# Kernel tuning notes

Measured on AMD Instinct MI355X. Metric: run time of the kernel, lower is better.

Reference implementation:

```python
import jax, jax.numpy as jnp
import numpy as np

B, S, D = 2, 2048, 2048
HK, HV = 16, 32
DK, DV = 128, 128
KDIM = HK * DK          # 2048
VDIM = HV * DV          # 4096
CONV_DIM = 2 * KDIM + VDIM  # 8192
KSIZE = 4
EPS = 1e-6


def setup_inputs() -> dict:
    key = jax.random.key(0)
    ks = jax.random.split(key, 10)
    w = lambda i, shape, sc=0.02: jax.random.normal(ks[i], shape, jnp.float32) * sc
    return {
        "hidden_states": jax.random.normal(ks[0], (B, S, D), jnp.float32),
        "w_qkv": w(1, (D, CONV_DIM)),
        "w_z": w(2, (D, VDIM)),
        "w_b": w(3, (D, HV)),
        "w_a": w(4, (D, HV)),
        "w_out": w(5, (VDIM, D)),
        "conv_w": w(6, (CONV_DIM, KSIZE), 0.2),   # depthwise conv kernel [C, K]
        "dt_bias": jnp.ones((HV,), jnp.float32),
        "A_log": jnp.log(jax.random.uniform(ks[7], (HV,), jnp.float32, 1e-3, 16.0)),
        "norm_weight": jnp.ones((DV,), jnp.float32),
    }


def _causal_conv1d(x, w):
    # x: [B,S,C], w: [C,K] depthwise; left-pad K-1 zeros -> causal, output len S
    xp = jnp.pad(x, ((0, 0), (KSIZE - 1, 0), (0, 0)))
    lhs = xp.transpose(0, 2, 1)            # [B,C,S+K-1]
    rhs = w[:, None, :]                    # [C,1,K]
    out = jax.lax.conv_general_dilated(lhs, rhs, (1,), 'VALID',
                                       feature_group_count=CONV_DIM)
    return out.transpose(0, 2, 1)          # [B,S,C]


def _l2norm(x, eps=1e-6):
    return x * jax.lax.rsqrt(jnp.sum(x * x, axis=-1, keepdims=True) + eps)


def _gated_delta_rule(q, k, v, g, beta):
    # q,k: [B,S,H,DK]; v: [B,S,H,DV]; g,beta: [B,S,H]
    q = q * (DK ** -0.5)

    def step(St, inp):
        q_t, k_t, v_t, g_t, b_t = inp      # [B,H,dk], [B,H,dk], [B,H,dv], [B,H], [B,H]
        St = St * jnp.exp(g_t)[..., None, None]             # per-head decay
        v_old = jnp.einsum('bhk,bhkv->bhv', k_t, St)        # read memory
        delta = (v_t - v_old) * b_t[..., None]              # delta-rule update
        St = St + k_t[..., None] * delta[:, :, None, :]     # write memory
        o = jnp.einsum('bhk,bhkv->bhv', q_t, St)            # read output
        return St, o

    tr = lambda x: jnp.moveaxis(x, 1, 0)  # seq-major for scan
    S0 = jnp.zeros((q.shape[0], HV, DK, DV), jnp.float32)
    _, out = jax.lax.scan(step, S0, (tr(q), tr(k), tr(v), tr(g), tr(beta)))
    return jnp.moveaxis(out, 0, 1)         # [B,S,H,DV]


def reference(hidden_states, w_qkv, w_z, w_b, w_a, w_out, conv_w,
              dt_bias, A_log, norm_weight):
    Bb, Ss, _ = hidden_states.shape
    mixed = hidden_states @ w_qkv                           # [B,S,CONV_DIM]
    z = (hidden_states @ w_z).reshape(Bb, Ss, HV, DV)
    b = hidden_states @ w_b                                 # [B,S,HV]
    a = hidden_states @ w_a                                 # [B,S,HV]

    mixed = jax.nn.silu(_causal_conv1d(mixed, conv_w))
    q, k, v = jnp.split(mixed, [KDIM, 2 * KDIM], axis=-1)
    q = _l2norm(q.reshape(Bb, Ss, HK, DK))
    k = _l2norm(k.reshape(Bb, Ss, HK, DK))
    v = v.reshape(Bb, Ss, HV, DV)

    beta = jax.nn.sigmoid(b)
    g = -jnp.exp(A_log) * jax.nn.softplus(a + dt_bias)      # [B,S,HV]

    rep = HV // HK
    q = jnp.repeat(q, rep, axis=2)
    k = jnp.repeat(k, rep, axis=2)

    core = _gated_delta_rule(q, k, v, g, beta)              # [B,S,HV,DV]

    # gated RMSNorm over DV: norm(x)*weight*silu(gate)
    var = jnp.mean(core * core, axis=-1, keepdims=True)
    core = core * jax.lax.rsqrt(var + EPS) * norm_weight
    core = core * jax.nn.silu(z)

    return core.reshape(Bb, Ss, VDIM) @ w_out               # [B,S,D]
```

## Files before the change

### kernel.cpp

```cpp
#include <hip/hip_runtime.h>
#include <hip/hip_bf16.h>
#include <cstdint>
#include <cstddef>


typedef __bf16 bf16;
typedef __bf16 bf16x8 __attribute__((ext_vector_type(8)));
typedef __bf16 bf16x4v __attribute__((ext_vector_type(4)));
typedef float f32x4 __attribute__((ext_vector_type(4)));

#define NB 2
#define NS 2048
#define ND 2048
#define NHK 16
#define NHV 32
#define NDK 128
#define NDV 128
#define NKDIM 2048
#define NVDIM 4096
#define NCONV 8192

__device__ __forceinline__ bool detect_f32(const void* dt_raw) {
  return ((const uint32_t*)dt_raw)[0] == 0x3F800000u;
}
__device__ __forceinline__ float inval(const void* p, size_t i, bool f32in) {
  return f32in ? ((const float*)p)[i] : (float)((const bf16*)p)[i];
}

__device__ __forceinline__ void gload_lds16(const bf16* gp, bf16* lp) {
  typedef __attribute__((address_space(1))) const void gvoid_t;
  typedef __attribute__((address_space(3))) void lvoid_t;
  __builtin_amdgcn_global_load_lds((gvoid_t*)gp, (lvoid_t*)lp, 16, 0, 0);
}

__global__ __launch_bounds__(256) void convert_hs(const void* __restrict__ in,
    const void* __restrict__ dt_raw, bf16* __restrict__ out)
{
  const bool f32in = detect_f32(dt_raw);
  const size_t base = (size_t)(blockIdx.x * 256 + threadIdx.x) * 8;
  bf16x8 o;
#pragma unroll
  for (int j = 0; j < 8; j++) o[j] = (bf16)inval(in, base + j, f32in);
  *(bf16x8*)(out + base) = o;
}

__global__ __launch_bounds__(256) void convert_small(const void* __restrict__ conv_w,
    const void* __restrict__ dt_bias, const void* __restrict__ A_log,
    const void* __restrict__ norm_w, bf16* __restrict__ conv_wB,
    float* __restrict__ dtf, float* __restrict__ alogf, float* __restrict__ normwf)
{
  const bool f32in = detect_f32(dt_bias);
  const int idx = blockIdx.x * 256 + threadIdx.x;
  if (idx < 32768)      conv_wB[idx] = (bf16)inval(conv_w, idx, f32in);
  else if (idx < 32800) dtf[idx - 32768]   = inval(dt_bias, idx - 32768, f32in);
  else if (idx < 32832) alogf[idx - 32800] = inval(A_log, idx - 32800, f32in);
  else if (idx < 32960) normwf[idx - 32832] = inval(norm_w, idx - 32832, f32in);
}

template <bool F32OUT>
__global__ __launch_bounds__(256) void gemm_bt(const bf16* __restrict__ A,
    const bf16* __restrict__ Bt, void* __restrict__ Cv, int M, int N, int K)
{
  __shared__ bf16 As[128 * 32];
  __shared__ bf16 Bs[128 * 32];
  const int tid  = threadIdx.x;
  const int lane = tid & 63;
  const int wave = tid >> 6;
  const int wr = wave >> 1, wc = wave & 1;
  const int l15 = lane & 15, quad = lane >> 4;
  const int bm = blockIdx.y * 128;
  const int bn = blockIdx.x * 128;

  f32x4 acc[4][4];
#pragma unroll
  for (int i = 0; i < 4; i++)
#pragma unroll
    for (int j = 0; j < 4; j++)
      acc[i][j] = (f32x4){0.f, 0.f, 0.f, 0.f};

  const int li0 = wave * 128 + lane;
  const int li1 = li0 + 64;
  const int r0 = li0 >> 2, c0 = (li0 & 3) * 8;
  const int r1 = li1 >> 2, c1 = (li1 & 3) * 8;

  for (int k0 = 0; k0 < K; k0 += 32) {
    gload_lds16(A  + (size_t)(bm + r0) * K + k0 + c0, &As[(wave * 2 + 0) * 512]);
    gload_lds16(A  + (size_t)(bm + r1) * K + k0 + c1, &As[(wave * 2 + 1) * 512]);
    gload_lds16(Bt + (size_t)(bn + r0) * K + k0 + c0, &Bs[(wave * 2 + 0) * 512]);
    gload_lds16(Bt + (size_t)(bn + r1) * K + k0 + c1, &Bs[(wave * 2 + 1) * 512]);
    __syncthreads();
    bf16x8 af[4], bfr[4];
#pragma unroll
    for (int mi = 0; mi < 4; mi++)
      af[mi] = *(const bf16x8*)&As[(wr * 64 + mi * 16 + l15) * 32 + quad * 8];
#pragma unroll
    for (int ni = 0; ni < 4; ni++)
      bfr[ni] = *(const bf16x8*)&Bs[(wc * 64 + ni * 16 + l15) * 32 + quad * 8];
#pragma unroll
    for (int mi = 0; mi < 4; mi++)
#pragma unroll
      for (int ni = 0; ni < 4; ni++)
        acc[mi][ni] = __builtin_amdgcn_mfma_f32_16x16x32_bf16(af[mi], bfr[ni], acc[mi][ni], 0, 0, 0);
    __syncthreads();
  }
#pragma unroll
  for (int mi = 0; mi < 4; mi++)
#pragma unroll
    for (int ni = 0; ni < 4; ni++)
#pragma unroll
      for (int r = 0; r < 4; r++) {
        const int row = bm + wr * 64 + mi * 16 + quad * 4 + r;
        const int col = bn + wc * 64 + ni * 16 + l15;
        if (F32OUT)
          ((float*)Cv)[(size_t)row * N + col] = acc[mi][ni][r];
        else
          ((bf16*)Cv)[(size_t)row * N + col] = (bf16)acc[mi][ni][r];
      }
}

__global__ __launch_bounds__(256) void transpose_k(const void* __restrict__ in,
    const void* __restrict__ dt_raw, bf16* __restrict__ out, int K, int N)
{
  const bool f32in = detect_f32(dt_raw);
  __shared__ bf16 tile[32][33];
  const int n0 = blockIdx.x * 32, k0 = blockIdx.y * 32;
  const int x = threadIdx.x, y0 = threadIdx.y;
#pragma unroll
  for (int i = 0; i < 4; i++) {
    int y = y0 + i * 8;
    tile[y][x] = (bf16)inval(in, (size_t)(k0 + y) * N + n0 + x, f32in);
  }
  __syncthreads();
#pragma unroll
  for (int i = 0; i < 4; i++) {
    int y = y0 + i * 8;
    out[(size_t)(n0 + y) * K + k0 + x] = tile[x][y];
  }
}

__global__ __launch_bounds__(256) void build_wba(const void* __restrict__ w_b,
    const void* __restrict__ w_a, const void* __restrict__ dt_raw,
    bf16* __restrict__ wbaT)
{
  const bool f32in = detect_f32(dt_raw);
  const int idx = blockIdx.x * 256 + threadIdx.x;
  const int n = idx >> 11, k = idx & 2047;
  bf16 v = (bf16)0.f;
  if (n < 32) v = (bf16)inval(w_b, (size_t)k * 32 + n, f32in);
  else if (n < 64) v = (bf16)inval(w_a, (size_t)k * 32 + (n - 32), f32in);
  wbaT[idx] = v;
}

__global__ __launch_bounds__(256) void betag_kernel(const bf16* __restrict__ ba,
    const float* __restrict__ dtf, const float* __restrict__ alogf,
    float* __restrict__ g, float* __restrict__ beta)
{
  const int idx = blockIdx.x * 256 + threadIdx.x;
  const int tok = idx >> 6, j = idx & 63;
  const float d = (float)ba[(size_t)tok * 128 + j];
  if (j < 32) {
    beta[(size_t)tok * 32 + j] = 1.f / (1.f + expf(-d));
  } else {
    const int h = j - 32;
    const float x = d + dtf[h];
    const float sp = (x > 20.f) ? x : log1pf(expf(x));
    g[(size_t)tok * 32 + h] = -expf(alogf[h]) * sp;
  }
}

__global__ __launch_bounds__(256) void conv_kernel(const bf16* __restrict__ mixed,
    const bf16* __restrict__ conv_w, bf16* __restrict__ qhat,
    bf16* __restrict__ khat, bf16* __restrict__ vout)
{
  const int blk = blockIdx.x;
  const int b = blk >> 11, s = blk & 2047;
  const int t = threadIdx.x;
  __shared__ float ssq[512];
  __shared__ float rn[32];
  float vals[4][8];
#pragma unroll
  for (int i = 0; i < 4; i++) {
    const int vg = t + 256 * i;
    const int c = vg * 8;
    const bf16x8* wp = (const bf16x8*)(conv_w + (size_t)c * 4);
    const bf16x8 w0 = wp[0], w1 = wp[1], w2 = wp[2], w3 = wp[3];
    float acc[8] = {0.f, 0.f, 0.f, 0.f, 0.f, 0.f, 0.f, 0.f};
#pragma unroll
    for (int l = 0; l < 4; l++) {
      const int ss = s - 3 + l;
      if (ss >= 0) {
        const bf16x8 x8 = *(const bf16x8*)(mixed + (size_t)(b * 2048 + ss) * NCONV + c);
#pragma unroll
        for (int j = 0; j < 8; j++) {
          const int widx = j * 4 + l;
          const float wv = (widx < 8)  ? (float)w0[widx]
                         : (widx < 16) ? (float)w1[widx - 8]
                         : (widx < 24) ? (float)w2[widx - 16]
                                       : (float)w3[widx - 24];
          acc[j] += (float)x8[j] * wv;
        }
      }
    }
    float lsq = 0.f;
#pragma unroll
    for (int j = 0; j < 8; j++) {
      const float x = acc[j];
      const float y = x / (1.f + expf(-x));
      vals[i][j] = y;
      lsq += y * y;
    }
    if (vg < 512) {
      ssq[vg] = lsq;
    } else {
      bf16x8 o;
#pragma unroll
      for (int j = 0; j < 8; j++) o[j] = (bf16)vals[i][j];
      *(bf16x8*)(vout + (size_t)(b * 2048 + s) * NVDIM + (c - 4096)) = o;
    }
  }
  __syncthreads();
  if (t < 32) {
    float sum = 0.f;
#pragma unroll
    for (int u = 0; u < 16; u++) sum += ssq[t * 16 + u];
    float r = rsqrtf(sum + 1e-6f);
    if (t < 16) r *= 0.08838834764831845f;
    rn[t] = r;
  }
  __syncthreads();
#pragma unroll
  for (int i = 0; i < 2; i++) {
    const int vg = t + 256 * i;
    const float sc = rn[vg >> 4];
    bf16x8 o;
#pragma unroll
    for (int j = 0; j < 8; j++) o[j] = (bf16)(vals[i][j] * sc);
    if (vg < 256)
      *(bf16x8*)(qhat + (size_t)(b * 2048 + s) * NKDIM + vg * 8) = o;
    else
      *(bf16x8*)(khat + (size_t)(b * 2048 + s) * NKDIM + (vg - 256) * 8) = o;
  }
}

__global__ __launch_bounds__(256) void prep_kernel(const bf16* __restrict__ qhat,
    const bf16* __restrict__ khat, bf16* __restrict__ vbuf,
    const float* __restrict__ g, const float* __restrict__ beta,
    bf16* __restrict__ Wg, bf16* __restrict__ Mg, float* __restrict__ egG,
    float* __restrict__ sc2G, float* __restrict__ egTotG)
{
  const int bid = blockIdx.x;
  const int c = bid & 127;
  const int h = (bid >> 7) & 31;
  const int b = bid >> 12;
  const int qh = h >> 1;
  const int s0 = c * 16;
  const int t = threadIdx.x;
  const int wave = t >> 6, lane = t & 63;
  const int l15 = lane & 15, quad = lane >> 4;
  const int sidx = t >> 4, seg = t & 15;

  __shared__ __attribute__((aligned(16))) bf16 pK[16 * 136];
  __shared__ __attribute__((aligned(16))) bf16 pQ[16 * 136];
  __shared__ __attribute__((aligned(16))) bf16 pV[16 * 136];
  __shared__ float sA[16 * 17];
  __shared__ float sGc[16], sEg[16], sBt[16];

  const f32x4 zero4 = (f32x4){0.f, 0.f, 0.f, 0.f};

  {
    const size_t kb = ((size_t)(b * 2048 + s0 + sidx) * NHK + qh) * NDK + seg * 8;
    *(bf16x8*)&pK[sidx * 136 + seg * 8] = *(const bf16x8*)(khat + kb);
    *(bf16x8*)&pQ[sidx * 136 + seg * 8] = *(const bf16x8*)(qhat + kb);
    const size_t vb = ((size_t)(b * 2048 + s0 + sidx) * NHV + h) * NDV + seg * 8;
    *(bf16x8*)&pV[sidx * 136 + seg * 8] = *(const bf16x8*)(vbuf + vb);
  }
  if (wave == 0) {
    float gb_r = 0.f;
    if (lane < 16)      gb_r = g[(size_t)(b * 2048 + s0 + lane) * NHV + h];
    else if (lane < 32) gb_r = beta[(size_t)(b * 2048 + s0 + (lane - 16)) * NHV + h];
    float gc = gb_r;
#pragma unroll
    for (int off = 1; off < 16; off <<= 1) {
      const float n = __shfl_up(gc, off);
      if ((lane & 15) >= off) gc += n;
    }
    const float gtot = __shfl(gc, 15);
    if (lane < 16) {
      sGc[lane] = gc;
      const float e = expf(gc);
      sEg[lane] = e;
      const float s2 = expf(gtot - gc);
      egG[(size_t)bid * 16 + lane] = e;
      sc2G[(size_t)bid * 16 + lane] = s2;
      if (lane == 15) egTotG[bid] = e;
    } else if (lane < 32) {
      sBt[lane - 16] = gb_r;
    }
  }
  __syncthreads();

  f32x4 accKK = zero4, accQK = zero4;
  if (wave == 0) {
#pragma unroll
    for (int kk = 0; kk < 4; kk++) {
      const bf16x8 af = *(const bf16x8*)&pK[l15 * 136 + kk * 32 + quad * 8];
      accKK = __builtin_amdgcn_mfma_f32_16x16x32_bf16(af, af, accKK, 0, 0, 0);
    }
#pragma unroll
    for (int r = 0; r < 4; r++) {
      const int tt = quad * 4 + r, ii = l15;
      float a = 0.f;
      if (ii < tt) a = sBt[tt] * expf(sGc[tt] - sGc[ii]) * accKK[r];
      sA[tt * 17 + ii] = a;
    }
  } else if (wave == 1) {
#pragma unroll
    for (int kk = 0; kk < 4; kk++) {
      const bf16x8 af = *(const bf16x8*)&pQ[l15 * 136 + kk * 32 + quad * 8];
      const bf16x8 bf_ = *(const bf16x8*)&pK[l15 * 136 + kk * 32 + quad * 8];
      accQK = __builtin_amdgcn_mfma_f32_16x16x32_bf16(af, bf_, accQK, 0, 0, 0);
    }
#pragma unroll
    for (int r = 0; r < 4; r++) {
      const int tt = quad * 4 + r, ii = l15;
      const float m = (ii <= tt) ? expf(sGc[tt] - sGc[ii]) * accQK[r] : 0.f;
      Mg[(size_t)bid * 512 + tt * 32 + ii] = (bf16)m;
      Mg[(size_t)bid * 512 + tt * 32 + 16 + ii] = (bf16)0.f;
    }
  }
  __syncthreads();

  {
    const int j = t;
    float x[16];
#pragma unroll
    for (int tt = 0; tt < 16; tt++) {
      float r = (j < 128) ? sBt[tt] * sEg[tt] * (float)pK[tt * 136 + j]
                          : sBt[tt] * (float)pV[tt * 136 + (j - 128)];
#pragma unroll
      for (int i = 0; i < 16; i++)
        if (i < tt) r = fmaf(-sA[tt * 17 + i], x[i], r);
      x[tt] = r;
    }
    if (j < 128) {
#pragma unroll
      for (int tt = 0; tt < 16; tt++)
        Wg[(size_t)bid * 2048 + tt * 128 + j] = (bf16)x[tt];
    } else {
#pragma unroll
      for (int tt = 0; tt < 16; tt++)
        vbuf[((size_t)(b * 2048 + s0 + tt) * NHV + h) * NDV + (j - 128)] = (bf16)x[tt];
    }
  }
}

__global__ __launch_bounds__(256, 2) void core_kernel(const bf16* __restrict__ qhat,
    const bf16* __restrict__ khat, const bf16* __restrict__ Ug,
    const bf16* __restrict__ Wg, const bf16* __restrict__ Mg,
    const float* __restrict__ egG, const float* __restrict__ sc2G,
    const float* __restrict__ egTotG, bf16* __restrict__ corep)
{
  const int bid = blockIdx.x;
  const int vblk = (bid & 7) * 64 + (bid >> 3);
  const int dvc = vblk & 7;
  const int h = (vblk >> 3) & 31;
  const int b = vblk >> 8;
  const int qh = h >> 1;
  const int dvbase = dvc * 16;
  const int t = threadIdx.x;
  const int wave = t >> 6, lane = t & 63;
  const int l15 = lane & 15, quad = lane >> 4;
  const int sidx = t >> 4, seg = t & 15;
  const size_t cb = (size_t)(b * 32 + h) * 128;

  __shared__ __attribute__((aligned(16))) bf16 sKb[2][16 * 136];
  __shared__ __attribute__((aligned(16))) bf16 sKT[128 * 40];
  __shared__ __attribute__((aligned(16))) bf16 sSt[2][16 * 136];
  __shared__ __attribute__((aligned(16))) bf16 sD[16 * 40];
  __shared__ __attribute__((aligned(16))) bf16 sD2[16 * 40];

  const f32x4 zero4 = (f32x4){0.f, 0.f, 0.f, 0.f};
  for (int i = t; i < 272; i += 256) {
    *(f32x4*)&sSt[0][i * 8] = zero4;
    *(f32x4*)&sSt[1][i * 8] = zero4;
  }
  for (int i = t; i < 80; i += 256) {
    *(f32x4*)&sD[i * 8] = zero4;
    *(f32x4*)&sD2[i * 8] = zero4;
  }
  for (int i = t; i < 640; i += 256) *(f32x4*)&sKT[i * 8] = zero4;

  f32x4 accS[2] = {zero4, zero4};

  const int swz = (l15 & 7) << 3;

  bf16x8 kv_r;
  bf16x8 wf[4]; float u4[4], sc2_4[4];
  bf16x8 qf[4], mf; float eg_4[4];
  float egTot_r;

  auto load_kv = [&](int c) {
    const int cc = c < 128 ? c : 127;
    kv_r = *(const bf16x8*)(khat +
        ((size_t)(b * 2048 + cc * 16 + sidx) * NHK + qh) * NDK + seg * 8);
  };
  auto load_w0 = [&](int c) {
    const int cc = c < 128 ? c : 127;
    const size_t wb = (cb + cc) * 2048 + (size_t)l15 * 128 + quad * 8;
#pragma unroll
    for (int kk = 0; kk < 4; kk++) wf[kk] = *(const bf16x8*)(Wg + wb + kk * 32);
#pragma unroll
    for (int r = 0; r < 4; r++) {
      u4[r] = (float)Ug[((size_t)(b * 2048 + cc * 16 + quad * 4 + r) * NHV + h) * NDV
                        + dvbase + l15];
      sc2_4[r] = sc2G[(cb + cc) * 16 + quad * 4 + r];
    }
  };
  auto load_qf = [&](int c) {
    const int cc = c < 128 ? c : 127;
    const size_t qb = ((size_t)(b * 2048 + cc * 16 + l15) * NHK + qh) * NDK + quad * 8;
#pragma unroll
    for (int kk = 0; kk < 4; kk++) qf[kk] = *(const bf16x8*)(qhat + qb + kk * 32);
  };
  auto load_w1m = [&](int c) {
    const int cc = c < 128 ? c : 127;
    mf = *(const bf16x8*)(Mg + (cb + cc) * 512 + l15 * 32 + quad * 8);
#pragma unroll
    for (int r = 0; r < 4; r++) eg_4[r] = egG[(cb + cc) * 16 + quad * 4 + r];
  };
  auto load_egtot = [&](int c) { egTot_r = egTotG[cb + (c < 128 ? c : 127)]; };

  load_kv(0);
  *(bf16x8*)&sKb[0][sidx * 136 + seg * 8] = kv_r;
  load_kv(1);
  if (wave == 0) load_w0(0);
  else if (wave == 1) { load_qf(0); load_w1m(0); }
  load_egtot(0);
  __syncthreads();

#pragma unroll 1
  for (int ch = 0; ch < 128; ++ch) {
    const int cur = ch & 1, nxt = cur ^ 1;
    const int s0 = ch * 16;
    f32x4 accO = zero4;
    if (wave == 0) {
      f32x4 aH = zero4, aL = zero4;
#pragma unroll
      for (int kk = 0; kk < 4; kk++) {
        const int col = (kk * 32 + quad * 8) ^ swz;
        const bf16x8 sh = *(const bf16x8*)&sSt[0][l15 * 136 + col];
        const bf16x8 sl = *(const bf16x8*)&sSt[1][l15 * 136 + col];
        aH = __builtin_amdgcn_mfma_f32_16x16x32_bf16(wf[kk], sh, aH, 0, 0, 0);
        aL = __builtin_amdgcn_mfma_f32_16x16x32_bf16(wf[kk], sl, aL, 0, 0, 0);
      }
      bf16x4v d4, d24;
#pragma unroll
      for (int r = 0; r < 4; r++) {
        const float d = u4[r] - (aH[r] + aL[r]);
        d4[r] = (bf16)d;
        d24[r] = (bf16)(d * sc2_4[r]);
      }
      *(bf16x4v*)&sD[l15 * 40 + quad * 4] = d4;
      *(bf16x4v*)&sD2[l15 * 40 + quad * 4] = d24;
      load_w0(ch + 1);
    } else if (wave == 1) {
      f32x4 aH = zero4, aL = zero4;
#pragma unroll
      for (int kk = 0; kk < 4; kk++) {
        const int col = (kk * 32 + quad * 8) ^ swz;
        const bf16x8 sh = *(const bf16x8*)&sSt[0][l15 * 136 + col];
        const bf16x8 sl = *(const bf16x8*)&sSt[1][l15 * 136 + col];
        aH = __builtin_amdgcn_mfma_f32_16x16x32_bf16(qf[kk], sh, aH, 0, 0, 0);
        aL = __builtin_amdgcn_mfma_f32_16x16x32_bf16(qf[kk], sl, aL, 0, 0, 0);
      }
#pragma unroll
      for (int r = 0; r < 4; r++) accO[r] = eg_4[r] * (aH[r] + aL[r]);
      load_qf(ch + 1);
    } else {
      const int dk_w = (wave - 2) * 64 + lane;
#pragma unroll
      for (int ih = 0; ih < 2; ih++) {
        bf16x8 kt;
#pragma unroll
        for (int j = 0; j < 8; j++) kt[j] = sKb[cur][(ih * 8 + j) * 136 + dk_w];
        *(bf16x8*)&sKT[dk_w * 40 + ih * 8] = kt;
      }
    }
    __syncthreads();
    *(bf16x8*)&sKb[nxt][sidx * 136 + seg * 8] = kv_r;
    load_kv(ch + 2);
    if (wave == 1) {
      const bf16x8 bD = *(const bf16x8*)&sD[l15 * 40 + quad * 8];
      accO = __builtin_amdgcn_mfma_f32_16x16x32_bf16(mf, bD, accO, 0, 0, 0);
#pragma unroll
      for (int r = 0; r < 4; r++)
        corep[((size_t)(b * 2048 + s0 + quad * 4 + r) * NHV + h) * NDV + dvbase + l15]
            = (bf16)accO[r];
      load_w1m(ch + 1);
    }
    {
      const bf16x8 bD2 = *(const bf16x8*)&sD2[l15 * 40 + quad * 8];
#pragma unroll
      for (int ti = 0; ti < 2; ti++) {
        const int dk0 = wave * 32 + ti * 16;
        const bf16x8 kf = *(const bf16x8*)&sKT[(dk0 + l15) * 40 + quad * 8];
        accS[ti] = accS[ti] * egTot_r;
        accS[ti] = __builtin_amdgcn_mfma_f32_16x16x32_bf16(kf, bD2, accS[ti], 0, 0, 0);
      }
      load_egtot(ch + 1);
#pragma unroll
      for (int ti = 0; ti < 2; ti++) {
        const int dk0 = wave * 32 + ti * 16;
        bf16x4v hi4, lo4;
#pragma unroll
        for (int r = 0; r < 4; r++) {
          const float v = accS[ti][r];
          const bf16 hi = (bf16)v;
          hi4[r] = hi;
          lo4[r] = (bf16)(v - (float)hi);
        }
        const int col = (dk0 + quad * 4) ^ swz;
        *(bf16x4v*)&sSt[0][l15 * 136 + col] = hi4;
        *(bf16x4v*)&sSt[1][l15 * 136 + col] = lo4;
      }
    }
    __syncthreads();
  }
}

__global__ __launch_bounds__(128) void normgate_kernel(const bf16* __restrict__ core,
    const bf16* __restrict__ z, const float* __restrict__ normwf,
    bf16* __restrict__ gated)
{
  const size_t idx = blockIdx.x;
  const int t = threadIdx.x;
  const float x = (float)core[idx * 128 + t];
  float p = x * x;
#pragma unroll
  for (int off = 32; off > 0; off >>= 1) p += __shfl_down(p, off);
  __shared__ float s2[2];
  if ((t & 63) == 0) s2[t >> 6] = p;
  __syncthreads();
  const float var = (s2[0] + s2[1]) * (1.f / 128.f);
  const float zv = (float)z[idx * 128 + t];
  const float y = x * rsqrtf(var + 1e-6f) * normwf[t] * (zv / (1.f + expf(-zv)));
  gated[idx * 128 + t] = (bf16)y;
}

extern "C" void kernel_launch(void* const* d_in, const int* in_sizes, int n_in,
                              void* d_out, int out_size, void* d_ws, size_t ws_size,
                              hipStream_t stream)
{
  const void* hs     = d_in[0];
  const void* w_qkv  = d_in[1];
  const void* w_z    = d_in[2];
  const void* w_b    = d_in[3];
  const void* w_a    = d_in[4];
  const void* w_out  = d_in[5];
  const void* conv_w = d_in[6];
  const void* dt_b   = d_in[7];
  const void* A_log  = d_in[8];
  const void* norm_w = d_in[9];

  char* ws = (char*)d_ws;
  bf16*  mixed = (bf16*)(ws + 0);
  bf16*  corep = (bf16*)(ws + 0);
  bf16*  Wg    = (bf16*)(ws + 33554432);
  bf16*  wqkvT = (bf16*)(ws + 67108864);
  bf16*  qhat  = (bf16*)(ws + 67108864);
  bf16*  khat  = (bf16*)(ws + 83886080);
  bf16*  gated = (bf16*)(ws + 67108864);
  bf16*  wzT   = (bf16*)(ws + 100663296);
  bf16*  woutT = (bf16*)(ws + 100663296);
  bf16*  vbuf  = (bf16*)(ws + 117440512);
  bf16*  zbuf  = (bf16*)(ws + 150994944);
  bf16*  hsB   = (bf16*)(ws + 184549376);
  bf16*  Mg    = (bf16*)(ws + 184549376);
  float* egG   = (float*)(ws + 192937984);
  float* sc2G  = (float*)(ws + 193462272);
  float* egTotG= (float*)(ws + 193986560);
  bf16*  wbaT  = (bf16*)(ws + 201326592);
  bf16*  ba    = (bf16*)(ws + 201850880);
  float* gb    = (float*)(ws + 202899456);
  float* betab = (float*)(ws + 203423744);
  bf16*  convwB= (bf16*)(ws + 203948032);
  float* dtf   = (float*)(ws + 204013568);
  float* alogf = (float*)(ws + 204013696);
  float* normwf= (float*)(ws + 204013824);

  convert_hs<<<4096, 256, 0, stream>>>(hs, dt_b, hsB);
  convert_small<<<129, 256, 0, stream>>>(conv_w, dt_b, A_log, norm_w,
                                         convwB, dtf, alogf, normwf);

  const dim3 tb(32, 8);
  transpose_k<<<dim3(NCONV / 32, ND / 32), tb, 0, stream>>>(w_qkv, dt_b, wqkvT, ND, NCONV);
  transpose_k<<<dim3(NVDIM / 32, ND / 32), tb, 0, stream>>>(w_z, dt_b, wzT, ND, NVDIM);
  build_wba<<<1024, 256, 0, stream>>>(w_b, w_a, dt_b, wbaT);

  gemm_bt<false><<<dim3(NCONV / 128, 32), 256, 0, stream>>>(hsB, wqkvT, mixed, 4096, NCONV, ND);
  gemm_bt<false><<<dim3(NVDIM / 128, 32), 256, 0, stream>>>(hsB, wzT, zbuf, 4096, NVDIM, ND);
  gemm_bt<false><<<dim3(1, 32), 256, 0, stream>>>(hsB, wbaT, ba, 4096, 128, ND);

  transpose_k<<<dim3(ND / 32, NVDIM / 32), tb, 0, stream>>>(w_out, dt_b, woutT, NVDIM, ND);

  betag_kernel<<<1024, 256, 0, stream>>>(ba, dtf, alogf, gb, betab);
  conv_kernel<<<NB * NS, 256, 0, stream>>>(mixed, convwB, qhat, khat, vbuf);
  prep_kernel<<<8192, 256, 0, stream>>>(qhat, khat, vbuf, gb, betab,
                                        Wg, Mg, egG, sc2G, egTotG);
  core_kernel<<<512, 256, 0, stream>>>(qhat, khat, vbuf, Wg, Mg,
                                       egG, sc2G, egTotG, corep);
  normgate_kernel<<<NB * NS * NHV, 128, 0, stream>>>(corep, zbuf, normwf, gated);

  gemm_bt<true><<<dim3(ND / 128, 32), 256, 0, stream>>>(gated, woutT, (void*)d_out, 4096, ND, NVDIM);
}
```

Measured before the change: 933.6 us.

## Replace projection GEMMs with 256x256-tile, 4-stage LDS-pipelined MFMA kernel

Adds a new GEMM kernel with 256x256 output tiles, 512 threads, a 4-deep buffer ring filled by direct global-to-LDS loads, an XCD-aware block remapping, and raised wave priority around the MFMA section. It replaces the old 128x128 GEMM for the qkv, z and output projections. The aim is more data reuse per tile and overlap of global loads with MFMA work. The larger LDS footprint and register tiles may limit occupancy, and the output projection grid has only 128 blocks, which may not fill the device.

```diff
diff --git a/kernel.cpp b/kernel.cpp
--- a/kernel.cpp
+++ b/kernel.cpp
@@ -55,6 +55,101 @@
   else if (idx < 32800) dtf[idx - 32768]   = inval(dt_bias, idx - 32768, f32in);
   else if (idx < 32832) alogf[idx - 32800] = inval(A_log, idx - 32800, f32in);
   else if (idx < 32960) normwf[idx - 32832] = inval(norm_w, idx - 32832, f32in);
+}
+
+template <bool F32OUT>
+__global__ __launch_bounds__(512, 2) void gemm256(const bf16* __restrict__ A,
+    const bf16* __restrict__ Bt, void* __restrict__ Cv, int M, int N, int K)
+{
+  const int nbx = N >> 8;
+  const int nwg = gridDim.x;
+  const int cpx = nwg >> 3;
+  const int wg = (blockIdx.x & 7) * cpx + (blockIdx.x >> 3);
+  const int bm = (wg / nbx) << 8;
+  const int bn = (wg % nbx) << 8;
+
+  const int t = threadIdx.x;
+  const int wave = t >> 6, lane = t & 63;
+  const int wm = wave >> 2, wn = wave & 3;
+  const int l15 = lane & 15, quad = lane >> 4;
+
+  __shared__ __attribute__((aligned(16))) bf16 sA[4][8192];
+  __shared__ __attribute__((aligned(16))) bf16 sB[4][8192];
+
+  const bf16* gA0 = A  + (size_t)(bm + (wave * 2 + 0) * 16 + l15) * K + quad * 8;
+  const bf16* gA1 = A  + (size_t)(bm + (wave * 2 + 1) * 16 + l15) * K + quad * 8;
+  const bf16* gB0 = Bt + (size_t)(bn + (wave * 2 + 0) * 16 + l15) * K + quad * 8;
+  const bf16* gB1 = Bt + (size_t)(bn + (wave * 2 + 1) * 16 + l15) * K + quad * 8;
+  const int sd0 = (wave * 2 + 0) * 512;
+  const int sd1 = (wave * 2 + 1) * 512;
+
+  auto STAGE = [&](int kt, int buf) {
+    const size_t off = (size_t)kt * 32;
+    gload_lds16(gA0 + off, &sA[buf][sd0]);
+    gload_lds16(gA1 + off, &sA[buf][sd1]);
+    gload_lds16(gB0 + off, &sB[buf][sd0]);
+    gload_lds16(gB1 + off, &sB[buf][sd1]);
+  };
+
+  f32x4 acc[8][4];
+#pragma unroll
+  for (int i = 0; i < 8; i++)
+#pragma unroll
+    for (int j = 0; j < 4; j++)
+      acc[i][j] = (f32x4){0.f, 0.f, 0.f, 0.f};
+
+  const int nkt = K >> 5;
+  const int frag = quad * 128 + l15 * 8;
+
+  STAGE(0, 0); STAGE(1, 1); STAGE(2, 2);
+  asm volatile("s_waitcnt vmcnt(8)" ::: "memory");
+  __builtin_amdgcn_s_barrier();
+  __builtin_amdgcn_sched_barrier(0);
+
+  for (int tt = 0; tt < nkt; ++tt) {
+    const int cur = tt & 3;
+    if (tt + 3 < nkt) STAGE(tt + 3, (tt + 3) & 3);
+
+    bf16x8 bfr[4];
+#pragma unroll
+    for (int ni = 0; ni < 4; ni++)
+      bfr[ni] = *(const bf16x8*)&sB[cur][(wn * 4 + ni) * 512 + frag];
+#pragma unroll
+    for (int h = 0; h < 2; h++) {
+      bf16x8 afr[4];
+#pragma unroll
+      for (int i = 0; i < 4; i++)
+        afr[i] = *(const bf16x8*)&sA[cur][(wm * 8 + h * 4 + i) * 512 + frag];
+      __builtin_amdgcn_s_setprio(1);
+#pragma unroll
+      for (int i = 0; i < 4; i++)
+#pragma unroll
+        for (int ni = 0; ni < 4; ni++)
+          acc[h * 4 + i][ni] = __builtin_amdgcn_mfma_f32_16x16x32_bf16(
+              afr[i], bfr[ni], acc[h * 4 + i][ni], 0, 0, 0);
+      __builtin_amdgcn_s_setprio(0);
+    }
+
+    if (tt < nkt - 3)       asm volatile("s_waitcnt vmcnt(8)" ::: "memory");
+    else if (tt == nkt - 3) asm volatile("s_waitcnt vmcnt(4)" ::: "memory");
+    else if (tt == nkt - 2) asm volatile("s_waitcnt vmcnt(0)" ::: "memory");
+    __builtin_amdgcn_s_barrier();
+    __builtin_amdgcn_sched_barrier(0);
+  }
+
+#pragma unroll
+  for (int mi = 0; mi < 8; mi++)
+#pragma unroll
+    for (int ni = 0; ni < 4; ni++)
+#pragma unroll
+      for (int r = 0; r < 4; r++) {
+        const int row = bm + wm * 128 + mi * 16 + quad * 4 + r;
+        const int col = bn + wn * 64 + ni * 16 + l15;
+        if (F32OUT)
+          ((float*)Cv)[(size_t)row * N + col] = acc[mi][ni][r];
+        else
+          ((bf16*)Cv)[(size_t)row * N + col] = (bf16)acc[mi][ni][r];
+      }
 }
 
 template <bool F32OUT>
@@ -597,8 +692,8 @@
   transpose_k<<<dim3(NVDIM / 32, ND / 32), tb, 0, stream>>>(w_z, dt_b, wzT, ND, NVDIM);
   build_wba<<<1024, 256, 0, stream>>>(w_b, w_a, dt_b, wbaT);
 
-  gemm_bt<false><<<dim3(NCONV / 128, 32), 256, 0, stream>>>(hsB, wqkvT, mixed, 4096, NCONV, ND);
-  gemm_bt<false><<<dim3(NVDIM / 128, 32), 256, 0, stream>>>(hsB, wzT, zbuf, 4096, NVDIM, ND);
+  gemm256<false><<<(NCONV / 256) * (4096 / 256), 512, 0, stream>>>(hsB, wqkvT, mixed, 4096, NCONV, ND);
+  gemm256<false><<<(NVDIM / 256) * (4096 / 256), 512, 0, stream>>>(hsB, wzT, zbuf, 4096, NVDIM, ND);
   gemm_bt<false><<<dim3(1, 32), 256, 0, stream>>>(hsB, wbaT, ba, 4096, 128, ND);
 
   transpose_k<<<dim3(ND / 32, NVDIM / 32), tb, 0, stream>>>(w_out, dt_b, woutT, NVDIM, ND);
@@ -611,5 +706,5 @@
                                        egG, sc2G, egTotG, corep);
   normgate_kernel<<<NB * NS * NHV, 128, 0, stream>>>(corep, zbuf, normwf, gated);
 
-  gemm_bt<true><<<dim3(ND / 128, 32), 256, 0, stream>>>(gated, woutT, (void*)d_out, 4096, ND, NVDIM);
-}
+  gemm256<true><<<(ND / 256) * (4096 / 256), 512, 0, stream>>>(gated, woutT, (void*)d_out, 4096, ND, NVDIM);
+}
```

After: 1.049 ms. 1.12x slower.
